# Kernel optimization log

Measured on AMD Instinct MI355X. Metric: run time of the kernel, lower is better.

Reference implementation:

```python
import jax, jax.numpy as jnp
import numpy as np

HEADS, HEAD_SIZE, FREQS, MAX_PERIOD = 16, 64, 256, 10000
D_MODEL = 1024
NEG_INF = -1e9


def sinusoid_embedding(seq_len, frequencies, max_period):
    # Interleaved sin/cos sinusoid table, shape (seq_len, frequencies).
    pos = np.arange(seq_len, dtype=np.float64)[:, None]
    idx = np.arange(frequencies)[None, :]
    inv_freq = max_period ** (-(idx // 2 * 2) / frequencies)
    angle = pos * inv_freq
    table = np.where(idx % 2 == 0, np.sin(angle), np.cos(angle))
    return table.astype(np.float32)


def relative_causal(scores):
    # scores: (b, n, q, v) with v indexing relative distance d = q - k.
    # Returns a[..., q, k] = scores[..., q, q - k] (k > q entries are masked later).
    L = scores.shape[-1]
    d = jnp.clip(jnp.arange(L)[:, None] - jnp.arange(L)[None, :], 0, L - 1)  # (q, k)
    return jnp.take_along_axis(scores, d[None, None, :, :], axis=-1)


def setup_inputs() -> dict:
    key = jax.random.key(0)
    ks = jax.random.split(key, 4)
    u = np.sqrt(3.0)
    inp = jax.random.normal(ks[0], (2, 2048, D_MODEL), dtype=jnp.float32)
    qkv = jax.random.uniform(ks[1], (D_MODEL, 3, HEADS, HEAD_SIZE), jnp.float32, -u, u)
    q_bias = jnp.zeros((HEADS, HEAD_SIZE), jnp.float32)
    positional = jax.random.uniform(ks[2], (FREQS, HEADS, HEAD_SIZE), jnp.float32, -u, u)
    out_kernel = jax.random.uniform(ks[3], (HEADS * HEAD_SIZE, D_MODEL), jnp.float32, -u, u)
    out_bias = jnp.zeros((D_MODEL,), jnp.float32)
    return {"input": inp, "qkv": qkv, "q_bias": q_bias, "positional": positional,
            "out_kernel": out_kernel, "out_bias": out_bias}


def reference(input, qkv, q_bias, positional, out_kernel, out_bias):
    b, s, x = input.shape
    n, h = HEADS, HEAD_SIZE
    # QKV projection with unit-scaling forward factor.
    w = qkv * (3.0 * x * h * n) ** -0.25
    q, k, v = jnp.einsum('bsx,xAnh->Abnsh', input, w)  # each (b, n, s, h)
    q = q + q_bias[:, None, :]
    # Content scores.
    a = jnp.einsum('bnqh,bnkh->bnqk', q, k) * h ** -0.5
    # Relative-positional scores (Transformer-XL style).
    sins = jnp.asarray(np.sqrt(2.0) * sinusoid_embedding(s, FREQS, MAX_PERIOD))
    emb = jnp.einsum('sf,fnh->nsh', sins, positional * FREQS ** -0.5)
    pos_scores = jnp.einsum('bnqh,nvh->bnqv', q, emb) * h ** -0.5
    a = a + relative_causal(pos_scores)
    # Causal mask + softmax.
    mask = jnp.tril(jnp.ones((s, s), dtype=bool))
    a = jax.nn.softmax(jnp.where(mask, a, NEG_INF), axis=-1)
    # Weighted sum and output projection (Dense, scale_for='both').
    o = jnp.einsum('bnqk,bnkh->bqnh', a, v).reshape(b, s, n * h)
    fan_in, fan_out = out_kernel.shape
    out = o @ (out_kernel * (fan_in * fan_out) ** -0.25) + out_bias
    return out
```

## Files before the change

### kernel.cpp

```cpp
#include <hip/hip_runtime.h>
#include <math.h>

#define BATCH 2
#define SEQ 2048
#define DMODEL 1024
#define HEADS 16
#define HSIZE 64
#define FREQS 256
#define NH 1024
#define QKVN 3072

typedef __bf16 bf16;
typedef __bf16 bf16x8 __attribute__((ext_vector_type(8)));
typedef float f32x4 __attribute__((ext_vector_type(4)));

static __device__ __forceinline__ unsigned short bf16_bits(float v) {
    bf16 b = (bf16)v; return __builtin_bit_cast(unsigned short, b);
}

static __device__ __forceinline__ void gload16(const void* g, void* l) {
    __builtin_amdgcn_global_load_lds(
        (const __attribute__((address_space(1))) unsigned int*)g,
        (__attribute__((address_space(3))) unsigned int*)l, 16, 0, 0);
}

__global__ __launch_bounds__(256) void prep_kernel(
    const float* __restrict__ inp, const float* __restrict__ qkv_w,
    const float* __restrict__ out_kernel, const float* __restrict__ positional,
    bf16* __restrict__ a_bf, bf16* __restrict__ wt_qkv,
    bf16* __restrict__ wt_out, bf16* __restrict__ wt_pos,
    bf16* __restrict__ sins_bf)
{
    __shared__ float tile[32][33];
    const int id = blockIdx.x, t = threadIdx.x;

    if (id < 4096) {
        int i = id * 256 + t;
        float4 v = ((const float4*)inp)[i];
        ushort4 o;
        o.x = bf16_bits(v.x); o.y = bf16_bits(v.y);
        o.z = bf16_bits(v.z); o.w = bf16_bits(v.w);
        ((ushort4*)a_bf)[i] = o;
        return;
    }
    if (id < 6144) {
        int i = (id - 4096) * 256 + t;
        int s = i >> 8, f = i & 255;
        double e = -(double)((f >> 1) << 1) / (double)FREQS;
        double invf = pow(10000.0, e);
        double ang = (double)s * invf;
        double v = (f & 1) ? cos(ang) : sin(ang);
        sins_bf[i] = (bf16)(float)(1.4142135623730951 * v);
        return;
    }
    int id2 = id - 6144;
    const float* src; bf16* dst; int R, C, c0, r0;
    if (id2 < 3072) {
        src = qkv_w; dst = wt_qkv; R = 1024; C = 3072;
        c0 = (id2 % 96) * 32; r0 = (id2 / 96) * 32;
    } else if (id2 < 4096) {
        id2 -= 3072;
        src = out_kernel; dst = wt_out; R = 1024; C = 1024;
        c0 = (id2 & 31) * 32; r0 = (id2 >> 5) * 32;
    } else {
        id2 -= 4096;
        src = positional; dst = wt_pos; R = 256; C = 1024;
        c0 = (id2 & 31) * 32; r0 = (id2 >> 5) * 32;
    }
    const int tx = t & 31, ty = t >> 5;
#pragma unroll
    for (int i = 0; i < 4; i++)
        tile[ty + i * 8][tx] = src[(size_t)(r0 + ty + i * 8) * C + c0 + tx];
    __syncthreads();
#pragma unroll
    for (int i = 0; i < 4; i++)
        dst[(size_t)(c0 + ty + i * 8) * R + r0 + tx] = (bf16)tile[tx][ty + i * 8];
}

template<int EPI>
__global__ __launch_bounds__(256) void mfma_gemm(
    const bf16* __restrict__ A, const bf16* __restrict__ Bt,
    int K, float alpha, const float* __restrict__ bias,
    float* __restrict__ outf, bf16* __restrict__ ob0, bf16* __restrict__ ob1,
    bf16* __restrict__ ob2,
    const bf16* __restrict__ A2, const bf16* __restrict__ Bt2,
    bf16* __restrict__ ob3, float alpha2)
{
    __shared__ __align__(16) bf16 Atile[2][128 * 32];
    __shared__ __align__(16) bf16 Btile[2][128 * 32];

    const int t    = threadIdx.x;
    const int lane = t & 63;
    const int w    = t >> 6;
    const int quad = lane >> 4;
    const int l16  = lane & 15;
    const int wm   = (w >> 1) * 64;
    const int wn   = (w & 1) * 64;

    bool embp = false;
    int m0 = blockIdx.y * 128, n0 = blockIdx.x * 128, Kl = K;
    const bf16* Ap = A; const bf16* Btp = Bt; float al = alpha;
    if constexpr (EPI == 1) {
        if (blockIdx.x >= 24) {
            if (blockIdx.y >= 16) return;
            embp = true;
            n0 = (blockIdx.x - 24) * 128;
            Kl = FREQS; Ap = A2; Btp = Bt2; al = alpha2;
        }
    }
    const bool swapv = (EPI == 1) && !embp && (n0 >= 2048);

    const int rS = t >> 2;
    const int cS = (t & 3) ^ ((rS >> 1) & 3);
    const bf16* ag0 = Ap  + (size_t)(m0 + rS) * Kl + cS * 8;
    const bf16* ag1 = ag0 + (size_t)64 * Kl;
    const bf16* bg0 = Btp + (size_t)(n0 + rS) * Kl + cS * 8;
    const bf16* bg1 = bg0 + (size_t)64 * Kl;

    int aoff[4], boff[4];
#pragma unroll
    for (int mi = 0; mi < 4; ++mi) {
        int r = wm + mi * 16 + l16;
        aoff[mi] = r * 32 + ((quad ^ ((r >> 1) & 3)) * 8);
    }
#pragma unroll
    for (int ni = 0; ni < 4; ++ni) {
        int r = wn + ni * 16 + l16;
        boff[ni] = r * 32 + ((quad ^ ((r >> 1) & 3)) * 8);
    }

    gload16(ag0, (char*)Atile[0] + t * 16);
    gload16(ag1, (char*)Atile[0] + 4096 + t * 16);
    gload16(bg0, (char*)Btile[0] + t * 16);
    gload16(bg1, (char*)Btile[0] + 4096 + t * 16);

    const int nK = Kl >> 5;
    f32x4 acc[4][4] = {};

    for (int kk = 0; kk < nK; ++kk) {
        __syncthreads();
        if (kk + 1 < nK) {
            ag0 += 32; ag1 += 32; bg0 += 32; bg1 += 32;
            char* ad = (char*)Atile[(kk + 1) & 1];
            char* bd = (char*)Btile[(kk + 1) & 1];
            gload16(ag0, ad + t * 16); gload16(ag1, ad + 4096 + t * 16);
            gload16(bg0, bd + t * 16); gload16(bg1, bd + 4096 + t * 16);
        }
        const bf16* ab = Atile[kk & 1];
        const bf16* bb = Btile[kk & 1];
        bf16x8 af[4], bfr[4];
#pragma unroll
        for (int mi = 0; mi < 4; ++mi) af[mi] = *(const bf16x8*)(ab + aoff[mi]);
#pragma unroll
        for (int ni = 0; ni < 4; ++ni) bfr[ni] = *(const bf16x8*)(bb + boff[ni]);

        if (!swapv) {
#pragma unroll
            for (int mi = 0; mi < 4; ++mi)
#pragma unroll
                for (int ni = 0; ni < 4; ++ni)
                    acc[mi][ni] = __builtin_amdgcn_mfma_f32_16x16x32_bf16(
                        af[mi], bfr[ni], acc[mi][ni], 0, 0, 0);
        } else {
#pragma unroll
            for (int mi = 0; mi < 4; ++mi)
#pragma unroll
                for (int ni = 0; ni < 4; ++ni)
                    acc[mi][ni] = __builtin_amdgcn_mfma_f32_16x16x32_bf16(
                        bfr[ni], af[mi], acc[mi][ni], 0, 0, 0);
        }
    }

    if constexpr (EPI == 0) {
#pragma unroll
        for (int mi = 0; mi < 4; ++mi)
#pragma unroll
            for (int ni = 0; ni < 4; ++ni) {
                int col = n0 + wn + ni * 16 + l16;
                float bb = bias[col];
#pragma unroll
                for (int rg = 0; rg < 4; ++rg) {
                    int row = m0 + wm + mi * 16 + quad * 4 + rg;
                    outf[(size_t)row * NH + col] = acc[mi][ni][rg] * al + bb;
                }
            }
    } else {
        if (embp) {
#pragma unroll
            for (int mi = 0; mi < 4; ++mi)
#pragma unroll
                for (int ni = 0; ni < 4; ++ni) {
                    int col = n0 + wn + ni * 16 + l16;
                    int head = col >> 6, h = col & 63;
#pragma unroll
                    for (int rg = 0; rg < 4; ++rg) {
                        int d = m0 + wm + mi * 16 + quad * 4 + rg;
                        int hs = h ^ (((d + 63) & 7) << 3);
                        ob3[((size_t)(head * SEQ + d)) * 64 + hs] =
                            (bf16)(acc[mi][ni][rg] * al);
                    }
                }
        } else if (n0 >= 2048) {
#pragma unroll
            for (int mi = 0; mi < 4; ++mi)
#pragma unroll
                for (int ni = 0; ni < 4; ++ni) {
                    int mcol = m0 + wm + mi * 16 + l16;
                    int bb = mcol >> 11, s = mcol & 2047;
#pragma unroll
                    for (int rg = 0; rg < 4; ++rg) {
                        int hg = n0 + wn + ni * 16 + quad * 4 + rg;
                        int head = (hg & 1023) >> 6, h = hg & 63;
                        int ss = s ^ ((h & 7) << 3);
                        ob2[((size_t)((bb * 16 + head) * 64 + h)) * SEQ + ss] =
                            (bf16)(acc[mi][ni][rg] * al);
                    }
                }
        } else {
            const int whichk = (n0 >= 1024);
#pragma unroll
            for (int mi = 0; mi < 4; ++mi)
#pragma unroll
                for (int ni = 0; ni < 4; ++ni) {
                    int cg   = (n0 + wn + ni * 16 + l16) & 1023;
                    int head = cg >> 6, h = cg & 63;
                    float qbv = whichk ? 0.0f : bias[cg];
#pragma unroll
                    for (int rg = 0; rg < 4; ++rg) {
                        int row = m0 + wm + mi * 16 + quad * 4 + rg;
                        int bb = row >> 11, s = row & 2047;
                        float v = acc[mi][ni][rg] * al;
                        if (whichk) {
                            int hs = h ^ ((s & 7) << 3);
                            ob1[((size_t)((bb * 16 + head) * SEQ + s)) * 64 + hs] = (bf16)v;
                        } else {
                            ob0[((size_t)((bb * 16 + head) * SEQ + s)) * 64 + h] =
                                (bf16)((v + qbv) * 0.125f);
                        }
                    }
                }
        }
    }
}

__global__ __launch_bounds__(256, 2) void attn_kernel(
    const bf16* __restrict__ Qb, const bf16* __restrict__ Kb,
    const bf16* __restrict__ Vtb, const bf16* __restrict__ Eb,
    bf16* __restrict__ o)
{
    __shared__ __align__(16) bf16 Ks[2][4096];
    __shared__ __align__(16) bf16 Vts[2][4096];
    __shared__ __align__(16) bf16 Es[256 * 64];
    __shared__ __align__(16) bf16 PS[4][16][72];

    const int t    = threadIdx.x;
    const int lane = t & 63;
    const int w    = t >> 6;
    const int quad = lane >> 4;
    const int l16  = lane & 15;

    const int bx = blockIdx.x;
    const int b  = bx >> 4, n = bx & 15;
    const int yy = blockIdx.y;
    const int qc = (yy < 8) ? (15 - 2 * yy) : (2 * yy - 16);
    const int q0 = qc * 128;
    const int KT = 2 * qc + 2;
    const int qw0 = q0 + 16 * w;
    const int qw1 = qw0 + 64;

    const bf16* __restrict__ Qp = Qb  + (size_t)bx * SEQ * 64;
    const bf16* __restrict__ Kp = Kb  + (size_t)bx * SEQ * 64;
    const bf16* __restrict__ Vp = Vtb + (size_t)bx * SEQ * 64;
    const bf16* __restrict__ Ep = Eb  + (size_t)n  * SEQ * 64;

    const int key8 = (l16 & 7) << 3;
    const int ec0  = ((quad * 8) ^ key8) * 2;
    const int ec1  = ((32 + quad * 8) ^ key8) * 2;

    bf16x8 qf[2][2];
    qf[0][0] = *(const bf16x8*)(Qp + (size_t)(qw0 + l16) * 64 + quad * 8);
    qf[0][1] = *(const bf16x8*)(Qp + (size_t)(qw0 + l16) * 64 + 32 + quad * 8);
    qf[1][0] = *(const bf16x8*)(Qp + (size_t)(qw1 + l16) * 64 + quad * 8);
    qf[1][1] = *(const bf16x8*)(Qp + (size_t)(qw1 + l16) * 64 + 32 + quad * 8);

    int dsta[4];
    bool condp[4];
#pragma unroll
    for (int rg = 0; rg < 4; ++rg) {
        int rr   = quad * 4 + rg;
        int l16c = (rr + 15 - l16) & 15;
        dsta[rg]  = ((lane & 48) + l16c) << 2;
        condp[rg] = rr > l16c;
    }

    f32x4 O[2][4] = {};
    float lsum[2][4] = {};

    {
        gload16(Kp + t * 8,        (char*)Ks[0] + t * 16);
        gload16(Kp + 2048 + t * 8, (char*)Ks[0] + 4096 + t * 16);
        gload16(Vp + (size_t)(t >> 3) * SEQ + (t & 7) * 8,        (char*)Vts[0] + t * 16);
        gload16(Vp + (size_t)((t >> 3) + 32) * SEQ + (t & 7) * 8, (char*)Vts[0] + 4096 + t * 16);
        const long D0 = (long)q0 - 63;
#pragma unroll
        for (int g = 0; g < 6; ++g)
            gload16(Ep + (D0 + 32 * g) * 64 + t * 8, (char*)Es + g * 4096 + t * 16);
    }

    for (int kt = 0; kt < KT; ++kt) {
        const int k0 = kt * 64;
        __syncthreads();

        const int nt = kt + 1;
        if (nt < KT) {
            bf16* kd = Ks[nt & 1];
            bf16* vd = Vts[nt & 1];
            const bf16* ksrc = Kp + nt * 4096;
            gload16(ksrc + t * 8,        (char*)kd + t * 16);
            gload16(ksrc + 2048 + t * 8, (char*)kd + 4096 + t * 16);
            gload16(Vp + (size_t)(t >> 3) * SEQ + nt * 64 + (t & 7) * 8,
                    (char*)vd + t * 16);
            gload16(Vp + (size_t)((t >> 3) + 32) * SEQ + nt * 64 + (t & 7) * 8,
                    (char*)vd + 4096 + t * 16);
            const long d0 = (long)q0 - nt * 64 - 63;
            const int rI = (-64 * nt) & 255;
            gload16(Ep + d0 * 64 + t * 8,        (char*)Es + rI * 128 + t * 16);
            gload16(Ep + (d0 + 32) * 64 + t * 8, (char*)Es + rI * 128 + 4096 + t * 16);
        }

        const char* kb = (const char*)Ks[kt & 1];
        const char* vb = (const char*)Vts[kt & 1];
        bf16x8 kf[4][2], vf[4][2];
#pragma unroll
        for (int j = 0; j < 4; ++j) {
            const char* kp = kb + (j * 16 + l16) * 128;
            kf[j][0] = *(const bf16x8*)(kp + ec0);
            kf[j][1] = *(const bf16x8*)(kp + ec1);
            const char* vp = vb + (j * 16 + l16) * 128;
            vf[j][0] = *(const bf16x8*)(vp + ec0);
            vf[j][1] = *(const bf16x8*)(vp + ec1);
        }

        const bool last = (nt == KT);
#pragma unroll
        for (int c = 0; c < 2; ++c) {
            if (c == 0 && last) continue;
            const int qwc = c ? qw1 : qw0;

            f32x4 pa[5];
            const int rb = 16 * w + 64 * c - k0;
#pragma unroll
            for (int jj = 0; jj < 5; ++jj) {
                const char* ep = (const char*)Es + ((rb + 16 * jj + l16) & 255) * 128;
                bf16x8 e0 = *(const bf16x8*)(ep + ec0);
                bf16x8 e1 = *(const bf16x8*)(ep + ec1);
                f32x4 a = {0, 0, 0, 0};
                a = __builtin_amdgcn_mfma_f32_16x16x32_bf16(qf[c][1], e1, a, 0, 0, 0);
                a = __builtin_amdgcn_mfma_f32_16x16x32_bf16(qf[c][0], e0, a, 0, 0, 0);
                pa[jj] = a;
            }

            f32x4 S[4];
#pragma unroll
            for (int j = 0; j < 4; ++j) {
                f32x4 a = {0, 0, 0, 0};
                a = __builtin_amdgcn_mfma_f32_16x16x32_bf16(qf[c][1], kf[j][1], a, 0, 0, 0);
                a = __builtin_amdgcn_mfma_f32_16x16x32_bf16(qf[c][0], kf[j][0], a, 0, 0, 0);
                S[j] = a;
            }

#pragma unroll
            for (int j = 0; j < 4; ++j) {
#pragma unroll
                for (int rg = 0; rg < 4; ++rg) {
                    float vsel = condp[rg] ? pa[4 - j][rg] : pa[3 - j][rg];
                    int pv = __builtin_amdgcn_ds_permute(dsta[rg], __float_as_int(vsel));
                    float sv = S[j][rg] + __int_as_float(pv);
                    bool valid = (k0 + j * 16 + l16) <= (qwc + quad * 4 + rg);
                    S[j][rg] = valid ? __expf(sv) : 0.0f;
                }
            }
#pragma unroll
            for (int rg = 0; rg < 4; ++rg)
                lsum[c][rg] += S[0][rg] + S[1][rg] + S[2][rg] + S[3][rg];

#pragma unroll
            for (int j = 0; j < 4; ++j)
#pragma unroll
                for (int rg = 0; rg < 4; ++rg)
                    PS[w][quad * 4 + rg][j * 16 + l16] = (bf16)S[j][rg];
            bf16x8 pf0 = *(const bf16x8*)(&PS[w][l16][quad * 8]);
            bf16x8 pf1 = *(const bf16x8*)(&PS[w][l16][32 + quad * 8]);

#pragma unroll
            for (int j4 = 0; j4 < 4; ++j4) {
                O[c][j4] = __builtin_amdgcn_mfma_f32_16x16x32_bf16(pf1, vf[j4][1], O[c][j4], 0, 0, 0);
                O[c][j4] = __builtin_amdgcn_mfma_f32_16x16x32_bf16(pf0, vf[j4][0], O[c][j4], 0, 0, 0);
            }
        }
    }

#pragma unroll
    for (int c = 0; c < 2; ++c) {
#pragma unroll
        for (int rg = 0; rg < 4; ++rg) {
            float s = lsum[c][rg];
            s += __shfl_xor(s, 1);
            s += __shfl_xor(s, 2);
            s += __shfl_xor(s, 4);
            s += __shfl_xor(s, 8);
            float inv = 1.0f / s;
            int q = (c ? qw1 : qw0) + quad * 4 + rg;
            size_t ro = ((size_t)(b * SEQ + q)) * NH + n * 64;
            o[ro +  0 + l16] = (bf16)(O[c][0][rg] * inv);
            o[ro + 16 + l16] = (bf16)(O[c][1][rg] * inv);
            o[ro + 32 + l16] = (bf16)(O[c][2][rg] * inv);
            o[ro + 48 + l16] = (bf16)(O[c][3][rg] * inv);
        }
    }
}

extern "C" void kernel_launch(void* const* d_in, const int* in_sizes, int n_in,
                              void* d_out, int out_size, void* d_ws, size_t ws_size,
                              hipStream_t stream) {
    const float* inp        = (const float*)d_in[0];
    const float* qkv_w      = (const float*)d_in[1];
    const float* q_bias     = (const float*)d_in[2];
    const float* positional = (const float*)d_in[3];
    const float* out_kernel = (const float*)d_in[4];
    const float* out_bias   = (const float*)d_in[5];

    char* p = (char*)d_ws;
    auto alloc = [&](size_t bytes) {
        char* q = p; p += (bytes + 255) & ~(size_t)255; return q;
    };
    bf16* qbuf    = (bf16*)alloc((size_t)BATCH * HEADS * SEQ * HSIZE * 2);
    bf16* kbuf    = (bf16*)alloc((size_t)BATCH * HEADS * SEQ * HSIZE * 2);
    bf16* vtbuf   = (bf16*)alloc((size_t)BATCH * HEADS * SEQ * HSIZE * 2);
    bf16* embT    = (bf16*)alloc((size_t)HEADS * SEQ * HSIZE * 2);
    bf16* sins_bf = (bf16*)alloc((size_t)SEQ * FREQS * 2);
    bf16* obuf    = (bf16*)alloc((size_t)BATCH * SEQ * NH * 2);
    bf16* a_bf    = (bf16*)alloc((size_t)BATCH * SEQ * DMODEL * 2);
    bf16* wt_qkv  = (bf16*)alloc((size_t)QKVN * DMODEL * 2);
    bf16* wt_out  = (bf16*)alloc((size_t)NH * DMODEL * 2);
    bf16* wt_pos  = (bf16*)alloc((size_t)NH * FREQS * 2);

    const float qkv_scale = (float)pow(3.0 * DMODEL * HSIZE * HEADS, -0.25);
    const float emb_scale = 0.0625f;
    const float out_scale = 0.03125f;

    prep_kernel<<<10496, 256, 0, stream>>>(
        inp, qkv_w, out_kernel, positional, a_bf, wt_qkv, wt_out, wt_pos, sins_bf);

    mfma_gemm<1><<<dim3(32, 32), 256, 0, stream>>>(
        a_bf, wt_qkv, DMODEL, qkv_scale, q_bias, nullptr, qbuf, kbuf, vtbuf,
        sins_bf, wt_pos, embT, emb_scale);

    attn_kernel<<<dim3(32, 16), 256, 0, stream>>>(
        qbuf, kbuf, vtbuf, embT, obuf);

    mfma_gemm<0><<<dim3(8, 32), 256, 0, stream>>>(
        obuf, wt_out, DMODEL, out_scale, out_bias, (float*)d_out,
        nullptr, nullptr, nullptr, nullptr, nullptr, nullptr, 0.0f);
}
```

Baseline: 263.0 us.

## Interleave the two query-chunk phases and peel the last KV tile

```diff
diff --git a/kernel.cpp b/kernel.cpp
--- a/kernel.cpp
+++ b/kernel.cpp
@@ -307,12 +307,85 @@
             gload16(Ep + (D0 + 32 * g) * 64 + t * 8, (char*)Es + g * 4096 + t * 16);
     }
 
-    for (int kt = 0; kt < KT; ++kt) {
+    auto load_kv = [&](const char* kb, const char* vb,
+                       bf16x8 (&kf)[4][2], bf16x8 (&vf)[4][2]) {
+#pragma unroll
+        for (int j = 0; j < 4; ++j) {
+            const char* kp = kb + (j * 16 + l16) * 128;
+            kf[j][0] = *(const bf16x8*)(kp + ec0);
+            kf[j][1] = *(const bf16x8*)(kp + ec1);
+            const char* vp = vb + (j * 16 + l16) * 128;
+            vf[j][0] = *(const bf16x8*)(vp + ec0);
+            vf[j][1] = *(const bf16x8*)(vp + ec1);
+        }
+    };
+    auto eread = [&](int rb, bf16x8 (&ef)[5][2]) {
+#pragma unroll
+        for (int jj = 0; jj < 5; ++jj) {
+            const char* ep = (const char*)Es + ((rb + 16 * jj + l16) & 255) * 128;
+            ef[jj][0] = *(const bf16x8*)(ep + ec0);
+            ef[jj][1] = *(const bf16x8*)(ep + ec1);
+        }
+    };
+    auto qkmfma = [&](const bf16x8 (&q2)[2], const bf16x8 (&kf)[4][2],
+                      f32x4 (&S)[4]) {
+#pragma unroll
+        for (int j = 0; j < 4; ++j) {
+            f32x4 a = {0, 0, 0, 0};
+            a = __builtin_amdgcn_mfma_f32_16x16x32_bf16(q2[1], kf[j][1], a, 0, 0, 0);
+            a = __builtin_amdgcn_mfma_f32_16x16x32_bf16(q2[0], kf[j][0], a, 0, 0, 0);
+            S[j] = a;
+        }
+    };
+    auto pamfma = [&](const bf16x8 (&q2)[2], const bf16x8 (&ef)[5][2],
+                      f32x4 (&pa)[5]) {
+#pragma unroll
+        for (int jj = 0; jj < 5; ++jj) {
+            f32x4 a = {0, 0, 0, 0};
+            a = __builtin_amdgcn_mfma_f32_16x16x32_bf16(q2[1], ef[jj][1], a, 0, 0, 0);
+            a = __builtin_amdgcn_mfma_f32_16x16x32_bf16(q2[0], ef[jj][0], a, 0, 0, 0);
+            pa[jj] = a;
+        }
+    };
+    auto smax = [&](int kq, f32x4 (&S)[4], const f32x4 (&pa)[5], float (&ls)[4]) {
+#pragma unroll
+        for (int j = 0; j < 4; ++j) {
+#pragma unroll
+            for (int rg = 0; rg < 4; ++rg) {
+                float vsel = condp[rg] ? pa[4 - j][rg] : pa[3 - j][rg];
+                int pv = __builtin_amdgcn_ds_permute(dsta[rg], __float_as_int(vsel));
+                float sv = S[j][rg] + __int_as_float(pv);
+                bool valid = (j * 16 + l16) <= (kq + quad * 4 + rg);
+                S[j][rg] = valid ? __expf(sv) : 0.0f;
+            }
+        }
+#pragma unroll
+        for (int rg = 0; rg < 4; ++rg)
+            ls[rg] += S[0][rg] + S[1][rg] + S[2][rg] + S[3][rg];
+    };
+    auto ps_write = [&](const f32x4 (&S)[4]) {
+#pragma unroll
+        for (int j = 0; j < 4; ++j)
+#pragma unroll
+            for (int rg = 0; rg < 4; ++rg)
+                PS[w][quad * 4 + rg][j * 16 + l16] = (bf16)S[j][rg];
+    };
+    auto pvmfma = [&](const bf16x8 (&vf)[4][2], f32x4 (&Oc)[4]) {
+        bf16x8 pf0 = *(const bf16x8*)(&PS[w][l16][quad * 8]);
+        bf16x8 pf1 = *(const bf16x8*)(&PS[w][l16][32 + quad * 8]);
+#pragma unroll
+        for (int j4 = 0; j4 < 4; ++j4) {
+            Oc[j4] = __builtin_amdgcn_mfma_f32_16x16x32_bf16(pf1, vf[j4][1], Oc[j4], 0, 0, 0);
+            Oc[j4] = __builtin_amdgcn_mfma_f32_16x16x32_bf16(pf0, vf[j4][0], Oc[j4], 0, 0, 0);
+        }
+    };
+
+    for (int kt = 0; kt < KT - 1; ++kt) {
         const int k0 = kt * 64;
         __syncthreads();
 
-        const int nt = kt + 1;
-        if (nt < KT) {
+        {
+            const int nt = kt + 1;
             bf16* kd = Ks[nt & 1];
             bf16* vd = Vts[nt & 1];
             const bf16* ksrc = Kp + nt * 4096;
@@ -328,76 +401,49 @@
             gload16(Ep + (d0 + 32) * 64 + t * 8, (char*)Es + rI * 128 + 4096 + t * 16);
         }
 
-        const char* kb = (const char*)Ks[kt & 1];
-        const char* vb = (const char*)Vts[kt & 1];
         bf16x8 kf[4][2], vf[4][2];
-#pragma unroll
-        for (int j = 0; j < 4; ++j) {
-            const char* kp = kb + (j * 16 + l16) * 128;
-            kf[j][0] = *(const bf16x8*)(kp + ec0);
-            kf[j][1] = *(const bf16x8*)(kp + ec1);
-            const char* vp = vb + (j * 16 + l16) * 128;
-            vf[j][0] = *(const bf16x8*)(vp + ec0);
-            vf[j][1] = *(const bf16x8*)(vp + ec1);
-        }
-
-        const bool last = (nt == KT);
-#pragma unroll
-        for (int c = 0; c < 2; ++c) {
-            if (c == 0 && last) continue;
-            const int qwc = c ? qw1 : qw0;
-
-            f32x4 pa[5];
-            const int rb = 16 * w + 64 * c - k0;
-#pragma unroll
-            for (int jj = 0; jj < 5; ++jj) {
-                const char* ep = (const char*)Es + ((rb + 16 * jj + l16) & 255) * 128;
-                bf16x8 e0 = *(const bf16x8*)(ep + ec0);
-                bf16x8 e1 = *(const bf16x8*)(ep + ec1);
-                f32x4 a = {0, 0, 0, 0};
-                a = __builtin_amdgcn_mfma_f32_16x16x32_bf16(qf[c][1], e1, a, 0, 0, 0);
-                a = __builtin_amdgcn_mfma_f32_16x16x32_bf16(qf[c][0], e0, a, 0, 0, 0);
-                pa[jj] = a;
-            }
-
-            f32x4 S[4];
-#pragma unroll
-            for (int j = 0; j < 4; ++j) {
-                f32x4 a = {0, 0, 0, 0};
-                a = __builtin_amdgcn_mfma_f32_16x16x32_bf16(qf[c][1], kf[j][1], a, 0, 0, 0);
-                a = __builtin_amdgcn_mfma_f32_16x16x32_bf16(qf[c][0], kf[j][0], a, 0, 0, 0);
-                S[j] = a;
-            }
-
-#pragma unroll
-            for (int j = 0; j < 4; ++j) {
-#pragma unroll
-                for (int rg = 0; rg < 4; ++rg) {
-                    float vsel = condp[rg] ? pa[4 - j][rg] : pa[3 - j][rg];
-                    int pv = __builtin_amdgcn_ds_permute(dsta[rg], __float_as_int(vsel));
-                    float sv = S[j][rg] + __int_as_float(pv);
-                    bool valid = (k0 + j * 16 + l16) <= (qwc + quad * 4 + rg);
-                    S[j][rg] = valid ? __expf(sv) : 0.0f;
-                }
-            }
-#pragma unroll
-            for (int rg = 0; rg < 4; ++rg)
-                lsum[c][rg] += S[0][rg] + S[1][rg] + S[2][rg] + S[3][rg];
-
-#pragma unroll
-            for (int j = 0; j < 4; ++j)
-#pragma unroll
-                for (int rg = 0; rg < 4; ++rg)
-                    PS[w][quad * 4 + rg][j * 16 + l16] = (bf16)S[j][rg];
-            bf16x8 pf0 = *(const bf16x8*)(&PS[w][l16][quad * 8]);
-            bf16x8 pf1 = *(const bf16x8*)(&PS[w][l16][32 + quad * 8]);
-
-#pragma unroll
-            for (int j4 = 0; j4 < 4; ++j4) {
-                O[c][j4] = __builtin_amdgcn_mfma_f32_16x16x32_bf16(pf1, vf[j4][1], O[c][j4], 0, 0, 0);
-                O[c][j4] = __builtin_amdgcn_mfma_f32_16x16x32_bf16(pf0, vf[j4][0], O[c][j4], 0, 0, 0);
-            }
-        }
+        load_kv((const char*)Ks[kt & 1], (const char*)Vts[kt & 1], kf, vf);
+
+        bf16x8 ef0[5][2];
+        eread(16 * w - k0, ef0);
+        f32x4 S0[4], pa0[5];
+        __builtin_amdgcn_s_setprio(1);
+        qkmfma(qf[0], kf, S0);
+        pamfma(qf[0], ef0, pa0);
+        __builtin_amdgcn_s_setprio(0);
+        smax(qw0 - k0, S0, pa0, lsum[0]);
+
+        bf16x8 ef1[5][2];
+        eread(16 * w + 64 - k0, ef1);
+        ps_write(S0);
+
+        f32x4 S1[4], pa1[5];
+        __builtin_amdgcn_s_setprio(1);
+        qkmfma(qf[1], kf, S1);
+        pamfma(qf[1], ef1, pa1);
+        pvmfma(vf, O[0]);
+        __builtin_amdgcn_s_setprio(0);
+
+        smax(qw1 - k0, S1, pa1, lsum[1]);
+        ps_write(S1);
+        __builtin_amdgcn_s_setprio(1);
+        pvmfma(vf, O[1]);
+        __builtin_amdgcn_s_setprio(0);
+    }
+
+    {
+        const int kt = KT - 1, k0 = kt * 64;
+        __syncthreads();
+        bf16x8 kf[4][2], vf[4][2];
+        load_kv((const char*)Ks[kt & 1], (const char*)Vts[kt & 1], kf, vf);
+        bf16x8 ef1[5][2];
+        eread(16 * w + 64 - k0, ef1);
+        f32x4 S1[4], pa1[5];
+        qkmfma(qf[1], kf, S1);
+        pamfma(qf[1], ef1, pa1);
+        smax(qw1 - k0, S1, pa1, lsum[1]);
+        ps_write(S1);
+        pvmfma(vf, O[1]);
     }
 
 #pragma unroll
```

Result: no change. 263.6 us (+0.2%).
